# Kernel tuning notes

Measured on AMD Instinct MI355X. Metric: run time of the kernel, lower is better.

The kernel has to match this reference:

```python
import jax, jax.numpy as jnp
import numpy as np
from jax import lax

B, T, S_ENC = 64, 32, 64
E, H, V = 1024, 1024, 32000


def setup_inputs() -> dict:
    key = jax.random.key(0)
    ks = jax.random.split(key, 12)
    s = 0.02
    return {
        "inputs": jax.random.randint(ks[0], (B, T), 0, V),
        "encoder_outputs": jax.random.normal(ks[1], (B, S_ENC, 2 * H), jnp.float32),
        "h0": jax.random.normal(ks[2], (B, H), jnp.float32) * 0.1,
        "c0": jax.random.normal(ks[3], (B, H), jnp.float32) * 0.1,
        "emb": jax.random.normal(ks[4], (V, E), jnp.float32) * s,
        "W_ih": jax.random.normal(ks[5], (4 * H, E), jnp.float32) * s,
        "W_hh": jax.random.normal(ks[6], (4 * H, H), jnp.float32) * s,
        "b_ih": jnp.zeros((4 * H,), jnp.float32),
        "b_hh": jnp.zeros((4 * H,), jnp.float32),
        "attn_W": jax.random.normal(ks[7], (2 * H, H), jnp.float32) * s,  # Linear(H -> 2H, no bias)
        "comb_W": jax.random.normal(ks[8], (H, 3 * H), jnp.float32) * s,  # Linear(3H -> H)
        "comb_b": jnp.zeros((H,), jnp.float32),
        "out_W": jax.random.normal(ks[9], (V, H), jnp.float32) * s,       # Linear(H -> V)
        "out_b": jnp.zeros((V,), jnp.float32),
    }


def _decode(inputs, encoder_outputs, h0, c0, emb, W_ih, W_hh, b_ih, b_hh,
            attn_W, comb_W, comb_b, out_W, out_b):
    x = emb[inputs]                      # [B, T, E]
    bias = b_ih + b_hh

    def step(carry, x_t):
        h, c = carry                     # [B, H] each
        gates = x_t @ W_ih.T + h @ W_hh.T + bias    # [B, 4H]
        i, f, g, o = jnp.split(gates, 4, axis=-1)   # PyTorch LSTM gate order
        i, f, o = jax.nn.sigmoid(i), jax.nn.sigmoid(f), jax.nn.sigmoid(o)
        c = f * c + i * jnp.tanh(g)
        h = o * jnp.tanh(c)
        # Luong-style attention (faithful to source, incl. softmax over dim=1 of size 1)
        ah = h @ attn_W.T                                        # [B, 2H]
        scores = jnp.einsum('bd,bsd->bs', ah, encoder_outputs)[:, None, :]  # [B,1,S]
        w = jax.nn.softmax(scores, axis=1)                       # size-1 axis -> all ones
        ctx = jnp.einsum('bqs,bsd->bqd', w, encoder_outputs)[:, 0]          # [B, 2H]
        merged = jnp.concatenate([h, ctx], axis=-1)              # [B, 3H]
        out = jnp.tanh(merged @ comb_W.T + comb_b)               # [B, H]
        return (h, c), out

    (h, c), outs = lax.scan(step, (h0, c0), x.transpose(1, 0, 2))
    outputs = outs.transpose(1, 0, 2)                            # [B, T, H]
    logits = outputs @ out_W.T + out_b                           # [B, T, V]
    return logits, h, c


def reference(inputs, encoder_outputs, h0, c0, emb, W_ih, W_hh, b_ih, b_hh,
              attn_W, comb_W, comb_b, out_W, out_b):
    return _decode(inputs, encoder_outputs, h0, c0, emb, W_ih, W_hh, b_ih, b_hh,
                   attn_W, comb_W, comb_b, out_W, out_b)
```

## Files before the change

### kernel.cpp

```cpp
#include <hip/hip_runtime.h>
#include <hip/hip_bf16.h>


typedef unsigned short u16;
typedef unsigned int u32;
typedef short s8v __attribute__((ext_vector_type(8)));
typedef float f4v __attribute__((ext_vector_type(4)));

__device__ __forceinline__ u16 f2bf(float f) {
  unsigned x = __float_as_uint(f);
  return (u16)((x + 0x7fffu + ((x >> 16) & 1u)) >> 16);
}
__device__ __forceinline__ float bf2f(u16 u) {
  return __uint_as_float(((unsigned)u) << 16);
}

__device__ __forceinline__ void gl_lds16(const void* g, void* l) {
  __builtin_amdgcn_global_load_lds(
      (const __attribute__((address_space(1))) u32*)g,
      (__attribute__((address_space(3))) u32*)l, 16, 0, 0);
}

__device__ __forceinline__ int xcd_swz(int bid, int nb) {
  int q8 = nb >> 3, r8 = nb & 7;
  int xcd = bid & 7, idx = bid >> 3;
  return (xcd < r8 ? xcd * (q8 + 1) : r8 * (q8 + 1) + (xcd - r8) * q8) + idx;
}

template <int EPI>
__global__ __launch_bounds__(256, 2) void gemm_bt2(
    const u16* __restrict__ A, const u16* __restrict__ Bm,
    const float* __restrict__ bias, void* __restrict__ Cp,
    int K, int ldc, int gridM) {
  __shared__ __align__(16) u16 As[128 * 64];
  __shared__ __align__(16) u16 Bs[128 * 64];

  int swz = xcd_swz((int)blockIdx.x, (int)gridDim.x);
  int mt = swz % gridM, nt = swz / gridM;
  long bm = (long)mt * 128, bn = (long)nt * 128;

  int tid = threadIdx.x;
  int w = tid >> 6, l = tid & 63;
  int wm = (w & 1) * 64, wn = (w >> 1) * 64;
  int lr = l & 15, lg = l >> 4;

  f4v acc[4][4];
#pragma unroll
  for (int i = 0; i < 4; ++i)
#pragma unroll
    for (int j = 0; j < 4; ++j) acc[i][j] = (f4v){0.f, 0.f, 0.f, 0.f};

  for (int kt = 0; kt < K; kt += 64) {
#pragma unroll
    for (int p = 0; p < 4; ++p) {
      int cb = (p * 4 + w) * 64;
      int c = cb + l;
      int row = c >> 3, ce = (c & 7) * 8;
      gl_lds16(A + (bm + row) * (long)K + kt + ce, &As[cb * 8]);
      gl_lds16(Bm + (bn + row) * (long)K + kt + ce, &Bs[cb * 8]);
    }
    __syncthreads();
#pragma unroll
    for (int ks = 0; ks < 2; ++ks) {
      int kb = ks * 64 + lg * 16;
      s8v av[4], bv[4];
#pragma unroll
      for (int i = 0; i < 4; ++i) {
        av[i] = *(const s8v*)((const char*)&As[0] + (wm + i * 16 + lr) * 128 + kb);
        bv[i] = *(const s8v*)((const char*)&Bs[0] + (wn + i * 16 + lr) * 128 + kb);
      }
#pragma unroll
      for (int mi = 0; mi < 4; ++mi)
#pragma unroll
        for (int ni = 0; ni < 4; ++ni)
          acc[mi][ni] = __builtin_amdgcn_mfma_f32_16x16x32_bf16(
              av[mi], bv[ni], acc[mi][ni], 0, 0, 0);
    }
    __syncthreads();
  }
#pragma unroll
  for (int mi = 0; mi < 4; ++mi) {
#pragma unroll
    for (int q = 0; q < 4; ++q) {
      long row = bm + wm + mi * 16 + lg * 4 + q;
#pragma unroll
      for (int ni = 0; ni < 4; ++ni) {
        long col = bn + wn + ni * 16 + lr;
        float v = acc[mi][ni][q] + bias[col];
        if (EPI == 2) v = tanhf(v);
        if (EPI == 3)
          ((float*)Cp)[row * (long)ldc + col] = v;
        else
          ((u16*)Cp)[row * (long)ldc + col] = f2bf(v);
      }
    }
  }
}

template <int EPI>
__global__ __launch_bounds__(256, 2) void gemm_btf(
    const u16* __restrict__ A, const float* __restrict__ Bm,
    const float* __restrict__ bias, void* __restrict__ Cp,
    int K, int ldc, int gridM) {
  __shared__ __align__(16) u16 As[128][72];
  __shared__ __align__(16) u16 Bs[128][72];
  int swz = xcd_swz((int)blockIdx.x, (int)gridDim.x);
  int mt = swz % gridM, nt = swz / gridM;
  long bm = (long)mt * 128, bn = (long)nt * 128;
  int tid = threadIdx.x;
  int w = tid >> 6, l = tid & 63;
  int wm = (w & 1) * 64, wn = (w >> 1) * 64;
  int lr = l & 15, lg = l >> 4;
  f4v acc[4][4];
#pragma unroll
  for (int i = 0; i < 4; ++i)
#pragma unroll
    for (int j = 0; j < 4; ++j) acc[i][j] = (f4v){0.f, 0.f, 0.f, 0.f};
  for (int kt = 0; kt < K; kt += 64) {
#pragma unroll
    for (int p = 0; p < 4; ++p) {
      int ch = p * 256 + tid;
      int row = ch >> 3, cc = ch & 7;
      *(uint4*)((char*)(&As[0][0]) + row * 144 + cc * 16) =
          *(const uint4*)(A + (bm + row) * (long)K + kt + cc * 8);
      const float* bp = Bm + (bn + row) * (long)K + kt + cc * 8;
      float4 b0 = *(const float4*)bp;
      float4 b1 = *(const float4*)(bp + 4);
      union { u16 t8[8]; uint4 v; } cv;
      cv.t8[0] = f2bf(b0.x); cv.t8[1] = f2bf(b0.y);
      cv.t8[2] = f2bf(b0.z); cv.t8[3] = f2bf(b0.w);
      cv.t8[4] = f2bf(b1.x); cv.t8[5] = f2bf(b1.y);
      cv.t8[6] = f2bf(b1.z); cv.t8[7] = f2bf(b1.w);
      *(uint4*)((char*)(&Bs[0][0]) + row * 144 + cc * 16) = cv.v;
    }
    __syncthreads();
#pragma unroll
    for (int ks = 0; ks < 2; ++ks) {
      int kb = ks * 64 + lg * 16;
      s8v av[4], bv[4];
#pragma unroll
      for (int i = 0; i < 4; ++i) {
        av[i] = *(const s8v*)((const char*)(&As[0][0]) + (wm + i * 16 + lr) * 144 + kb);
        bv[i] = *(const s8v*)((const char*)(&Bs[0][0]) + (wn + i * 16 + lr) * 144 + kb);
      }
#pragma unroll
      for (int mi = 0; mi < 4; ++mi)
#pragma unroll
        for (int ni = 0; ni < 4; ++ni)
          acc[mi][ni] = __builtin_amdgcn_mfma_f32_16x16x32_bf16(
              av[mi], bv[ni], acc[mi][ni], 0, 0, 0);
    }
    __syncthreads();
  }
#pragma unroll
  for (int mi = 0; mi < 4; ++mi) {
#pragma unroll
    for (int q = 0; q < 4; ++q) {
      long row = bm + wm + mi * 16 + lg * 4 + q;
#pragma unroll
      for (int ni = 0; ni < 4; ++ni) {
        long col = bn + wn + ni * 16 + lr;
        float v = acc[mi][ni][q] + bias[col];
        if (EPI == 2) v = tanhf(v);
        if (EPI == 3)
          ((float*)Cp)[row * (long)ldc + col] = v;
        else
          ((u16*)Cp)[row * (long)ldc + col] = f2bf(v);
      }
    }
  }
}

__global__ __launch_bounds__(256, 1) void lstm_step3(
    const u16* __restrict__ Whh, const u16* __restrict__ xproj,
    const u16* __restrict__ h_in, u16* __restrict__ h_next,
    float* __restrict__ c_buf, u16* __restrict__ a2,
    float* __restrict__ hf, float* __restrict__ cf, int t) {
  __shared__ __align__(16) u16 Hs[32 * 1024];
  __shared__ __align__(16) u16 Ws[32 * 1024];
  __shared__ float Gs[32][33];

  int bid = blockIdx.x;
  int j = bid & 127, bh = bid >> 7;
  int colbase = j * 8;
  int tid = threadIdx.x, w = tid >> 6, l = tid & 63;
  int bq = w & 1, nh = w >> 1;
  int lr = l & 15, lg = l >> 4;

  int hi = tid >> 7;
  int ps = tid & 127;
#pragma unroll
  for (int p = 0; p < 16; ++p) {
    int r = 2 * p + hi;
    int sl = ps ^ (r & 7);
    gl_lds16(h_in + (bh * 32 + r) * 1024 + sl * 8, &Hs[(p * 4 + w) * 512]);
    int g = r >> 3, rr = r & 7;
    gl_lds16(Whh + (long)(g * 1024 + colbase + rr) * 1024 + sl * 8,
             &Ws[(p * 4 + w) * 512]);
  }
  __syncthreads();

  int ar = bq * 16 + lr;
  int br = nh * 16 + lr;
  int axor = (ar & 7), bxor = (br & 7);
  f4v acc0 = {0.f, 0.f, 0.f, 0.f}, acc1 = {0.f, 0.f, 0.f, 0.f};
#pragma unroll
  for (int kc = 0; kc < 32; kc += 2) {
    {
      int s = kc * 4 + lg;
      s8v av = *(const s8v*)((const char*)Hs + ar * 2048 + (s ^ axor) * 16);
      s8v bv = *(const s8v*)((const char*)Ws + br * 2048 + (s ^ bxor) * 16);
      acc0 = __builtin_amdgcn_mfma_f32_16x16x32_bf16(av, bv, acc0, 0, 0, 0);
    }
    {
      int s = (kc + 1) * 4 + lg;
      s8v av = *(const s8v*)((const char*)Hs + ar * 2048 + (s ^ axor) * 16);
      s8v bv = *(const s8v*)((const char*)Ws + br * 2048 + (s ^ bxor) * 16);
      acc1 = __builtin_amdgcn_mfma_f32_16x16x32_bf16(av, bv, acc1, 0, 0, 0);
    }
  }
#pragma unroll
  for (int q = 0; q < 4; ++q)
    Gs[bq * 16 + lg * 4 + q][nh * 16 + lr] = acc0[q] + acc1[q];
  __syncthreads();

  int b = tid >> 3, rr = tid & 7;
  int gb = bh * 32 + b;
  int col = colbase + rr;
  const u16* xp = xproj + (long)(gb * 32 + t) * 4096;
  float pi = Gs[b][rr]      + bf2f(xp[col]);
  float pf = Gs[b][8 + rr]  + bf2f(xp[1024 + col]);
  float pg = Gs[b][16 + rr] + bf2f(xp[2048 + col]);
  float po = Gs[b][24 + rr] + bf2f(xp[3072 + col]);
  float iv = 1.f / (1.f + expf(-pi));
  float fv = 1.f / (1.f + expf(-pf));
  float ov = 1.f / (1.f + expf(-po));
  float gv = tanhf(pg);
  float co = c_buf[gb * 1024 + col];
  float cn = fv * co + iv * gv;
  float hn = ov * tanhf(cn);
  c_buf[gb * 1024 + col] = cn;
  u16 hb = f2bf(hn);
  h_next[gb * 1024 + col] = hb;
  a2[(long)(gb * 32 + t) * 3072 + col] = hb;
  if (t == 31) {
    hf[gb * 1024 + col] = hn;
    cf[gb * 1024 + col] = cn;
  }
}

__global__ void k_misc(const float* __restrict__ bih, const float* __restrict__ bhh,
                       const float* __restrict__ h0, const float* __restrict__ c0,
                       float* __restrict__ bias, u16* __restrict__ hbuf0,
                       float* __restrict__ cbuf) {
  int i = blockIdx.x * 256 + threadIdx.x;
  if (i < 4096) bias[i] = bih[i] + bhh[i];
  if (i < 65536) {
    hbuf0[i] = f2bf(h0[i]);
    cbuf[i] = c0[i];
  }
}

__global__ void k_cvt8(const float* __restrict__ src, u16* __restrict__ dst, int n8) {
  int i = blockIdx.x * 256 + threadIdx.x;
  if (i >= n8) return;
  const float4* s = (const float4*)(src + (long)i * 8);
  float4 a = s[0], b = s[1];
  union { u16 t[8]; uint4 v; } cv;
  cv.t[0] = f2bf(a.x); cv.t[1] = f2bf(a.y); cv.t[2] = f2bf(a.z); cv.t[3] = f2bf(a.w);
  cv.t[4] = f2bf(b.x); cv.t[5] = f2bf(b.y); cv.t[6] = f2bf(b.z); cv.t[7] = f2bf(b.w);
  ((uint4*)dst)[i] = cv.v;
}

__global__ void k_emb8(const int* __restrict__ inp, const float* __restrict__ emb,
                       u16* __restrict__ dst) {
  int i = blockIdx.x * 256 + threadIdx.x;
  int r = i >> 7, k8 = (i & 127) * 8;
  const float* s = emb + (long)inp[r] * 1024 + k8;
  float4 a = *(const float4*)s, b = *(const float4*)(s + 4);
  union { u16 t[8]; uint4 v; } cv;
  cv.t[0] = f2bf(a.x); cv.t[1] = f2bf(a.y); cv.t[2] = f2bf(a.z); cv.t[3] = f2bf(a.w);
  cv.t[4] = f2bf(b.x); cv.t[5] = f2bf(b.y); cv.t[6] = f2bf(b.z); cv.t[7] = f2bf(b.w);
  ((uint4*)dst)[i] = cv.v;
}

__global__ void k_ctx2(const float* __restrict__ enc, u16* __restrict__ a2) {
  int b = blockIdx.x;
  int dg = threadIdx.x;
  float s[8] = {0.f, 0.f, 0.f, 0.f, 0.f, 0.f, 0.f, 0.f};
  for (int si = 0; si < 64; ++si) {
    const float* p = enc + ((long)(b * 64 + si)) * 2048 + dg * 8;
    float4 x = *(const float4*)p, y = *(const float4*)(p + 4);
    s[0] += x.x; s[1] += x.y; s[2] += x.z; s[3] += x.w;
    s[4] += y.x; s[5] += y.y; s[6] += y.z; s[7] += y.w;
  }
  union { u16 t[8]; uint4 v; } cv;
#pragma unroll
  for (int e = 0; e < 8; ++e) cv.t[e] = f2bf(s[e]);
  for (int t = 0; t < 32; ++t)
    *(uint4*)(a2 + (long)(b * 32 + t) * 3072 + 1024 + dg * 8) = cv.v;
}

extern "C" void kernel_launch(void* const* d_in, const int* in_sizes, int n_in,
                              void* d_out, int out_size, void* d_ws, size_t ws_size,
                              hipStream_t stream) {
  (void)in_sizes; (void)n_in; (void)out_size;
  const int*   inputs = (const int*)d_in[0];
  const float* enc    = (const float*)d_in[1];
  const float* h0     = (const float*)d_in[2];
  const float* c0     = (const float*)d_in[3];
  const float* emb    = (const float*)d_in[4];
  const float* Wih    = (const float*)d_in[5];
  const float* Whh    = (const float*)d_in[6];
  const float* bih    = (const float*)d_in[7];
  const float* bhh    = (const float*)d_in[8];
  const float* combW  = (const float*)d_in[10];
  const float* combb  = (const float*)d_in[11];
  const float* outW   = (const float*)d_in[12];
  const float* outb   = (const float*)d_in[13];
  float* out = (float*)d_out;

  char* ws = (char*)d_ws;
  size_t off = 0;
  auto alloc = [&](size_t bytes) {
    char* p = ws + off;
    off += (bytes + 255) & ~(size_t)255;
    return p;
  };
  u16*   WHH_BF = (u16*)  alloc(4096ull * 1024 * 2);
  u16*   XPROJ  = (u16*)  alloc(2048ull * 4096 * 2);
  u16*   EMBX   = (u16*)  alloc(2048ull * 1024 * 2);
  u16*   A2     = (u16*)  alloc(2048ull * 3072 * 2);
  u16*   OUTS   = (u16*)  alloc(2048ull * 1024 * 2);
  float* BIAS   = (float*)alloc(4096 * 4);
  u16*   HBUF   = (u16*)  alloc(2ull * 65536 * 2);
  float* CBUF   = (float*)alloc(65536 * 4);
  u16*   WIH_BF   = (u16*)alloc(4096ull * 1024 * 2);
  u16*   COMBW_BF = (u16*)alloc(1024ull * 3072 * 2);
  size_t off_w1 = off;
  u16*   OUTW_BF  = (u16*)alloc(32000ull * 1024 * 2);
  size_t off_w2 = off;
  bool haveW1 = ws_size >= off_w1;
  bool haveW2 = ws_size >= off_w2;

  k_misc<<<dim3(256), dim3(256), 0, stream>>>(bih, bhh, h0, c0, BIAS, HBUF, CBUF);
  k_cvt8<<<dim3(2048), dim3(256), 0, stream>>>(Whh, WHH_BF, 524288);
  k_emb8<<<dim3(1024), dim3(256), 0, stream>>>(inputs, emb, EMBX);
  k_ctx2<<<dim3(64), dim3(256), 0, stream>>>(enc, A2);
  if (haveW1) {
    k_cvt8<<<dim3(2048), dim3(256), 0, stream>>>(Wih, WIH_BF, 524288);
    k_cvt8<<<dim3(1536), dim3(256), 0, stream>>>(combW, COMBW_BF, 393216);
  }
  if (haveW2)
    k_cvt8<<<dim3(16000), dim3(256), 0, stream>>>(outW, OUTW_BF, 4096000);

  if (haveW1)
    gemm_bt2<1><<<dim3(512), dim3(256), 0, stream>>>(EMBX, WIH_BF, BIAS, XPROJ,
                                                     1024, 4096, 16);
  else
    gemm_btf<1><<<dim3(512), dim3(256), 0, stream>>>(EMBX, Wih, BIAS, XPROJ,
                                                     1024, 4096, 16);

  for (int t = 0; t < 32; ++t) {
    u16* hin  = HBUF + (t & 1) * 65536;
    u16* hout = HBUF + ((t + 1) & 1) * 65536;
    lstm_step3<<<dim3(256), dim3(256), 0, stream>>>(
        WHH_BF, XPROJ, hin, hout, CBUF, A2,
        out + 65536000, out + 65536000 + 65536, t);
  }

  if (haveW1)
    gemm_bt2<2><<<dim3(128), dim3(256), 0, stream>>>(A2, COMBW_BF, combb, OUTS,
                                                     3072, 1024, 16);
  else
    gemm_btf<2><<<dim3(128), dim3(256), 0, stream>>>(A2, combW, combb, OUTS,
                                                     3072, 1024, 16);
  if (haveW2)
    gemm_bt2<3><<<dim3(4000), dim3(256), 0, stream>>>(OUTS, OUTW_BF, outb, d_out,
                                                      1024, 32000, 16);
  else
    gemm_btf<3><<<dim3(4000), dim3(256), 0, stream>>>(OUTS, outW, outb, d_out,
                                                      1024, 32000, 16);
}
```

Baseline: 627.3 us.

## Add triple-buffered 128x256 GEMM kernel for input projection and vocab projection

```diff
diff --git a/kernel.cpp b/kernel.cpp
--- a/kernel.cpp
+++ b/kernel.cpp
@@ -25,6 +25,111 @@
   int q8 = nb >> 3, r8 = nb & 7;
   int xcd = bid & 7, idx = bid >> 3;
   return (xcd < r8 ? xcd * (q8 + 1) : r8 * (q8 + 1) + (xcd - r8) * q8) + idx;
+}
+
+template <int EPI>
+__global__ __launch_bounds__(512, 1) void gemm_p(
+    const u16* __restrict__ A, const u16* __restrict__ Bm,
+    const float* __restrict__ bias, void* __restrict__ Cp,
+    int K, int ldc, int gridM) {
+  __shared__ __align__(16) u16 LDS[3 * 24576];
+
+  int swz = xcd_swz((int)blockIdx.x, (int)gridDim.x);
+  int mt = swz % gridM, nt = swz / gridM;
+  long bm = (long)mt * 128, bn = (long)nt * 256;
+
+  int tid = threadIdx.x;
+  int w = tid >> 6, l = tid & 63;
+  int wm = w & 1, wn = w >> 1;
+  int lr = l & 15, lg = l >> 4;
+
+  int nt_k = K >> 6;
+
+  auto stage = [&](int s, int kt_idx) {
+    int kt = kt_idx << 6;
+    u16* sa = &LDS[s * 24576];
+    u16* sb = &LDS[s * 24576 + 8192];
+#pragma unroll
+    for (int ch = 0; ch < 2; ++ch) {
+      int cb = ch * 512 + w * 64;
+      int c = cb + l;
+      int row = c >> 3, sp = c & 7;
+      gl_lds16(A + (bm + row) * (long)K + kt + ((sp ^ (row & 7)) << 3),
+               sa + cb * 8);
+    }
+#pragma unroll
+    for (int ch = 0; ch < 4; ++ch) {
+      int cb = ch * 512 + w * 64;
+      int c = cb + l;
+      int row = c >> 3, sp = c & 7;
+      gl_lds16(Bm + (bn + row) * (long)K + kt + ((sp ^ (row & 7)) << 3),
+               sb + cb * 8);
+    }
+  };
+
+  f4v acc[4][4];
+#pragma unroll
+  for (int i = 0; i < 4; ++i)
+#pragma unroll
+    for (int j = 0; j < 4; ++j) acc[i][j] = (f4v){0.f, 0.f, 0.f, 0.f};
+
+  stage(0, 0);
+  stage(1, 1);
+  asm volatile("s_waitcnt vmcnt(6)" ::: "memory");
+  __builtin_amdgcn_s_barrier();
+  __builtin_amdgcn_sched_barrier(0);
+
+  for (int t = 0; t < nt_k; ++t) {
+    if (t + 2 < nt_k) stage((t + 2) % 3, t + 2);
+    const u16* sa = &LDS[(t % 3) * 24576];
+    const u16* sb = &LDS[(t % 3) * 24576 + 8192];
+#pragma unroll
+    for (int ks = 0; ks < 2; ++ks) {
+      s8v av[4], bv[4];
+#pragma unroll
+      for (int i = 0; i < 4; ++i) {
+        int ra = wm * 64 + i * 16 + lr;
+        int pa = (ks * 4 + lg) ^ (ra & 7);
+        av[i] = *(const s8v*)((const char*)sa + ra * 128 + pa * 16);
+        int rb = wn * 64 + i * 16 + lr;
+        int pb = (ks * 4 + lg) ^ (rb & 7);
+        bv[i] = *(const s8v*)((const char*)sb + rb * 128 + pb * 16);
+      }
+      __builtin_amdgcn_s_setprio(1);
+#pragma unroll
+      for (int mi = 0; mi < 4; ++mi)
+#pragma unroll
+        for (int ni = 0; ni < 4; ++ni)
+          acc[mi][ni] = __builtin_amdgcn_mfma_f32_16x16x32_bf16(
+              av[mi], bv[ni], acc[mi][ni], 0, 0, 0);
+      __builtin_amdgcn_s_setprio(0);
+    }
+    if (t + 1 >= nt_k) break;
+    if (t + 2 < nt_k) {
+      asm volatile("s_waitcnt vmcnt(6)" ::: "memory");
+    } else {
+      asm volatile("s_waitcnt vmcnt(0)" ::: "memory");
+    }
+    __builtin_amdgcn_s_barrier();
+    __builtin_amdgcn_sched_barrier(0);
+  }
+
+#pragma unroll
+  for (int mi = 0; mi < 4; ++mi) {
+#pragma unroll
+    for (int q = 0; q < 4; ++q) {
+      long row = bm + wm * 64 + mi * 16 + lg * 4 + q;
+#pragma unroll
+      for (int ni = 0; ni < 4; ++ni) {
+        long col = bn + wn * 64 + ni * 16 + lr;
+        float v = acc[mi][ni][q] + bias[col];
+        if (EPI == 3)
+          ((float*)Cp)[row * (long)ldc + col] = v;
+        else
+          ((u16*)Cp)[row * (long)ldc + col] = f2bf(v);
+      }
+    }
+  }
 }
 
 template <int EPI>
@@ -355,8 +460,8 @@
     k_cvt8<<<dim3(16000), dim3(256), 0, stream>>>(outW, OUTW_BF, 4096000);
 
   if (haveW1)
-    gemm_bt2<1><<<dim3(512), dim3(256), 0, stream>>>(EMBX, WIH_BF, BIAS, XPROJ,
-                                                     1024, 4096, 16);
+    gemm_p<1><<<dim3(256), dim3(512), 0, stream>>>(EMBX, WIH_BF, BIAS, XPROJ,
+                                                   1024, 4096, 16);
   else
     gemm_btf<1><<<dim3(512), dim3(256), 0, stream>>>(EMBX, Wih, BIAS, XPROJ,
                                                      1024, 4096, 16);
@@ -376,8 +481,8 @@
     gemm_btf<2><<<dim3(128), dim3(256), 0, stream>>>(A2, combW, combb, OUTS,
                                                      3072, 1024, 16);
   if (haveW2)
-    gemm_bt2<3><<<dim3(4000), dim3(256), 0, stream>>>(OUTS, OUTW_BF, outb, d_out,
-                                                      1024, 32000, 16);
+    gemm_p<3><<<dim3(2000), dim3(512), 0, stream>>>(OUTS, OUTW_BF, outb, d_out,
+                                                    1024, 32000, 16);
   else
     gemm_btf<3><<<dim3(4000), dim3(256), 0, stream>>>(OUTS, outW, outb, d_out,
                                                       1024, 32000, 16);
```

Measured after the change: 599.3 us. -4.5%, faster.
